# Kernel tuning notes

Measured on AMD Instinct MI355X. Metric: run time of the kernel, lower is better.

Reference implementation:

```python
import jax, jax.numpy as jnp
import numpy as np

B, T, L, V = 2048, 256, 32, 128
BLANK = V - 1          # Keras/TF CTC uses last class as blank
EPS = 1e-7             # keras backend epsilon used in ctc_batch_cost's log
NEG = -1e30            # log-space -inf surrogate (fp-safe)


def setup_inputs() -> dict:
    key = jax.random.key(0)
    k1, k2 = jax.random.split(key)
    # y_pred are softmax posteriors, as ctc_batch_cost expects
    logits = jax.random.normal(k1, (B, T, V), dtype=jnp.float32)
    y_pred = jax.nn.softmax(logits, axis=-1)
    # labels exclude the blank class (V-1)
    y_true = jax.random.randint(k2, (B, L), 0, BLANK, dtype=jnp.int64)
    return {"y_true": y_true, "y_pred": y_pred}


def _ctc_loss(y_true, y_pred):
    Bb, Tt, Vv = y_pred.shape
    Ll = y_true.shape[1]
    S = 2 * Ll + 1  # extended label length: blank-interleaved

    # extended labels: [blank, l1, blank, l2, ..., lL, blank]  -> [B, S]
    ext = jnp.full((Bb, S), BLANK, dtype=y_true.dtype).at[:, 1::2].set(y_true)

    logp = jnp.log(y_pred + EPS)  # [B, T, V], matches K.ctc_batch_cost
    # gather per-frame log-probs of each extended-label symbol: [B, T, S]
    lp_ext = jnp.take_along_axis(
        logp, jnp.broadcast_to(ext[:, None, :], (Bb, Tt, S)), axis=2
    )

    # skip transition (s-2 -> s) allowed iff ext[s] != blank and ext[s] != ext[s-2]
    ext_m2 = jnp.pad(ext, ((0, 0), (2, 0)), constant_values=-1)[:, :S]
    skip = (ext != BLANK) & (ext != ext_m2)  # [B, S]

    # alpha init at t=0: only first blank and first label reachable
    alpha0 = (
        jnp.full((Bb, S), NEG, dtype=logp.dtype)
        .at[:, 0].set(lp_ext[:, 0, 0])
        .at[:, 1].set(lp_ext[:, 0, 1])
    )

    def step(alpha, lp_t):
        # alpha: [B, S], lp_t: [B, S]
        s1 = jnp.pad(alpha, ((0, 0), (1, 0)), constant_values=NEG)[:, :S]
        s2 = jnp.pad(alpha, ((0, 0), (2, 0)), constant_values=NEG)[:, :S]
        a = jnp.logaddexp(alpha, s1)
        a = jnp.logaddexp(a, jnp.where(skip, s2, NEG))
        return a + lp_t, None

    lp_ts = jnp.transpose(lp_ext, (1, 0, 2))[1:]  # [T-1, B, S]
    alphaT, _ = jax.lax.scan(step, alpha0, lp_ts)

    # total log-likelihood = logsumexp over last blank and last label states
    loss = -jnp.logaddexp(alphaT[:, S - 1], alphaT[:, S - 2])  # [B]
    return loss[:, None]  # K.ctc_batch_cost returns [B, 1]


def reference(y_true, y_pred):
    return _ctc_loss(y_true, y_pred)
```

## Files before the change

kernel.cpp:

```cpp
#include <hip/hip_runtime.h>


constexpr int Bb = 2048;
constexpr int Tt = 256;
constexpr int Ll = 32;
constexpr int Vv = 128;
constexpr int BLANK = Vv - 1;
constexpr int PF = 16;
#define EPSF 1e-7f
#define NEGF -1e30f
#define LN2F 0.6931471805599453f

__device__ __forceinline__ float fexp2(float x) { return __builtin_amdgcn_exp2f(x); }
__device__ __forceinline__ float flog2(float x) { return __builtin_amdgcn_logf(x); }
__device__ __forceinline__ float rdlane(float v, int l) {
    return __uint_as_float(__builtin_amdgcn_readlane(__float_as_uint(v), l));
}
__device__ __forceinline__ float dpp_shr1(float old, float src) {
    return __int_as_float(__builtin_amdgcn_update_dpp(
        __float_as_int(old), __float_as_int(src), 0x138 ,
        0xf, 0xf, false));
}

__global__ __launch_bounds__(256) void ctc_fwd(const int* __restrict__ y_true,
                                               const float* __restrict__ y_pred,
                                               float* __restrict__ out) {
    const int w    = blockIdx.x * 4 + (threadIdx.x >> 6);
    const int lane = threadIdx.x & 63;

    int sym = BLANK;
    if (!(lane & 1)) sym = y_true[w * Ll + (lane >> 1)];
    const int  symm2 = __shfl_up(sym, 2);
    const bool skip  = !(lane & 1) && (lane >= 2) && (sym != symm2);

    const float* rp = y_pred + (size_t)w * Tt * Vv + sym;

    const float lp20 = flog2(rp[0] + EPSF);
    float b0 = rdlane(lp20, 1);
    float m  = (lane == 0) ? lp20 : NEGF;
    float p  = 1.0f;
    const float negv = NEGF;
    const float onev = 1.0f;

    auto step = [&](float prob) {
        const float lp2  = flog2(prob + EPSF);
        const float lpb  = rdlane(lp2, 1);
        const float b0p  = b0;
        const float m1g = dpp_shr1(b0p,  m);
        const float p1g = dpp_shr1(onev, p);
        const float m2s = dpp_shr1(negv, m1g);
        const float p2g = dpp_shr1(onev, p1g);
        const float m2g = skip ? m2s : NEGF;
        const float hi  = fmaxf(fmaxf(m, m1g), m2g);
        const float pn  = p   * fexp2(m   - hi)
                        + p1g * fexp2(m1g - hi)
                        + p2g * fexp2(m2g - hi);
        m  = hi + lp2;
        p  = pn;
        b0 = b0p + lpb;
    };
    auto renorm = [&]() {
        m += flog2(fmaxf(p, 1e-30f));  p = 1.0f;
    };

    float buf[PF];
#pragma unroll
    for (int i = 0; i < PF; ++i) buf[i] = rp[(size_t)(1 + i) * Vv];

    for (int tb = 1; tb + PF <= Tt; tb += PF) {
#pragma unroll
        for (int i = 0; i < PF; ++i) {
            const float pr = buf[i];
            const int   tn = tb + i + PF;
            if (tn < Tt) buf[i] = rp[(size_t)tn * Vv];
            step(pr);
            if ((i & 7) == 7) renorm();
        }
    }
#pragma unroll
    for (int i = 0; i < PF - 1; ++i) {
        step(buf[i]);
        if (i == 7) renorm();
    }

    const float afin = m + flog2(fmaxf(p, 1e-30f));
    const float aA = rdlane(afin, 62);
    const float aB = rdlane(afin, 63);
    if (lane == 0) {
        const float h = fmaxf(aA, aB);
        const float r = h + flog2(fexp2(aA - h) + fexp2(aB - h));
        out[w] = -r * LN2F;
    }
}

extern "C" void kernel_launch(void* const* d_in, const int* in_sizes, int n_in,
                              void* d_out, int out_size, void* d_ws, size_t ws_size,
                              hipStream_t stream) {
    const int*   y_true = (const int*)d_in[0];
    const float* y_pred = (const float*)d_in[1];
    float*       out    = (float*)d_out;
    ctc_fwd<<<dim3(Bb / 4), dim3(256), 0, stream>>>(y_true, y_pred, out);
}
```

Measured before the change: 47.66 us.

## Split each sequence into producer and consumer waves with an LDS double buffer

Each block now handles one batch element with two waves. Wave 0 loads the posteriors, takes their log2 and writes 16-frame chunks into a double-buffered LDS array. Wave 1 reads each chunk after a barrier and runs only the DPP-based alpha recurrence. The aim is to take global-load latency and the log computation off the serial recurrence path. In exchange the kernel launches twice as many waves, half of which do no recurrence work, and adds a block barrier per chunk.

```diff
diff --git a/kernel.cpp b/kernel.cpp
--- a/kernel.cpp
+++ b/kernel.cpp
@@ -6,7 +6,8 @@
 constexpr int Ll = 32;
 constexpr int Vv = 128;
 constexpr int BLANK = Vv - 1;
-constexpr int PF = 16;
+constexpr int CHUNK = 16;
+constexpr int NCH = Tt / CHUNK;
 #define EPSF 1e-7f
 #define NEGF -1e30f
 #define LN2F 0.6931471805599453f
@@ -22,74 +23,99 @@
         0xf, 0xf, false));
 }
 
-__global__ __launch_bounds__(256) void ctc_fwd(const int* __restrict__ y_true,
+__global__ __launch_bounds__(128) void ctc_fwd(const int* __restrict__ y_true,
                                                const float* __restrict__ y_pred,
                                                float* __restrict__ out) {
-    const int w    = blockIdx.x * 4 + (threadIdx.x >> 6);
+    const int w    = blockIdx.x;
+    const int wave = threadIdx.x >> 6;
     const int lane = threadIdx.x & 63;
+
+    __shared__ float buf[2][CHUNK][64];
 
     int sym = BLANK;
     if (!(lane & 1)) sym = y_true[w * Ll + (lane >> 1)];
-    const int  symm2 = __shfl_up(sym, 2);
-    const bool skip  = !(lane & 1) && (lane >= 2) && (sym != symm2);
 
-    const float* rp = y_pred + (size_t)w * Tt * Vv + sym;
+    if (wave == 0) {
+        const float* rp = y_pred + (size_t)w * Tt * Vv + sym;
+        float rA[CHUNK], rB[CHUNK];
+#pragma unroll
+        for (int i = 0; i < CHUNK; ++i) rA[i] = rp[(size_t)i * Vv];
+        for (int cc = 0; cc < NCH / 2; ++cc) {
+            const int c0 = 2 * cc, c1 = 2 * cc + 1;
+#pragma unroll
+            for (int i = 0; i < CHUNK; ++i)
+                rB[i] = rp[(size_t)(c1 * CHUNK + i) * Vv];
+#pragma unroll
+            for (int i = 0; i < CHUNK; ++i)
+                buf[0][i][lane] = flog2(rA[i] + EPSF);
+            __syncthreads();
+            if (c1 + 1 < NCH) {
+#pragma unroll
+                for (int i = 0; i < CHUNK; ++i)
+                    rA[i] = rp[(size_t)((c1 + 1) * CHUNK + i) * Vv];
+            }
+#pragma unroll
+            for (int i = 0; i < CHUNK; ++i)
+                buf[1][i][lane] = flog2(rB[i] + EPSF);
+            __syncthreads();
+        }
+    } else {
+        const int  symm2 = __shfl_up(sym, 2);
+        const bool skip  = !(lane & 1) && (lane >= 2) && (sym != symm2);
 
-    const float lp20 = flog2(rp[0] + EPSF);
-    float b0 = rdlane(lp20, 1);
-    float m  = (lane == 0) ? lp20 : NEGF;
-    float p  = 1.0f;
-    const float negv = NEGF;
-    const float onev = 1.0f;
+        float m = NEGF, p = 1.0f, b0 = 0.0f;
 
-    auto step = [&](float prob) {
-        const float lp2  = flog2(prob + EPSF);
-        const float lpb  = rdlane(lp2, 1);
-        const float b0p  = b0;
-        const float m1g = dpp_shr1(b0p,  m);
-        const float p1g = dpp_shr1(onev, p);
-        const float m2s = dpp_shr1(negv, m1g);
-        const float p2g = dpp_shr1(onev, p1g);
-        const float m2g = skip ? m2s : NEGF;
-        const float hi  = fmaxf(fmaxf(m, m1g), m2g);
-        const float pn  = p   * fexp2(m   - hi)
-                        + p1g * fexp2(m1g - hi)
-                        + p2g * fexp2(m2g - hi);
-        m  = hi + lp2;
-        p  = pn;
-        b0 = b0p + lpb;
-    };
-    auto renorm = [&]() {
-        m += flog2(fmaxf(p, 1e-30f));  p = 1.0f;
-    };
+        auto step = [&](float lp2) {
+            const float lpb = rdlane(lp2, 1);
+            const float b0p = b0;
+            const float m1g = dpp_shr1(b0p,  m);
+            const float p1g = dpp_shr1(1.0f, p);
+            const float m2s = dpp_shr1(NEGF, m1g);
+            const float p2g = dpp_shr1(1.0f, p1g);
+            const float m2g = skip ? m2s : NEGF;
+            const float hi  = fmaxf(fmaxf(m, m1g), m2g);
+            const float pn  = p   * fexp2(m   - hi)
+                            + p1g * fexp2(m1g - hi)
+                            + p2g * fexp2(m2g - hi);
+            m  = hi + lp2;
+            p  = pn;
+            b0 = b0p + lpb;
+        };
+        auto renorm = [&]() {
+            m += flog2(fmaxf(p, 1e-30f));  p = 1.0f;
+        };
 
-    float buf[PF];
+        for (int c = 0; c < NCH; ++c) {
+            __syncthreads();
+            float lp[CHUNK];
 #pragma unroll
-    for (int i = 0; i < PF; ++i) buf[i] = rp[(size_t)(1 + i) * Vv];
+            for (int i = 0; i < CHUNK; ++i) lp[i] = buf[c & 1][i][lane];
+            if (c == 0) {
+                b0 = rdlane(lp[0], 1);
+                m  = (lane == 0) ? lp[0] : NEGF;
+                p  = 1.0f;
+#pragma unroll
+                for (int i = 1; i < CHUNK; ++i) {
+                    step(lp[i]);
+                    if ((i & 7) == 7) renorm();
+                }
+            } else {
+#pragma unroll
+                for (int i = 0; i < CHUNK; ++i) {
+                    step(lp[i]);
+                    if ((i & 7) == 7) renorm();
+                }
+            }
+        }
 
-    for (int tb = 1; tb + PF <= Tt; tb += PF) {
-#pragma unroll
-        for (int i = 0; i < PF; ++i) {
-            const float pr = buf[i];
-            const int   tn = tb + i + PF;
-            if (tn < Tt) buf[i] = rp[(size_t)tn * Vv];
-            step(pr);
-            if ((i & 7) == 7) renorm();
+        const float afin = m + flog2(fmaxf(p, 1e-30f));
+        const float aA = rdlane(afin, 62);
+        const float aB = rdlane(afin, 63);
+        if (lane == 0) {
+            const float h = fmaxf(aA, aB);
+            const float r = h + flog2(fexp2(aA - h) + fexp2(aB - h));
+            out[w] = -r * LN2F;
         }
-    }
-#pragma unroll
-    for (int i = 0; i < PF - 1; ++i) {
-        step(buf[i]);
-        if (i == 7) renorm();
-    }
-
-    const float afin = m + flog2(fmaxf(p, 1e-30f));
-    const float aA = rdlane(afin, 62);
-    const float aB = rdlane(afin, 63);
-    if (lane == 0) {
-        const float h = fmaxf(aA, aB);
-        const float r = h + flog2(fexp2(aA - h) + fexp2(aB - h));
-        out[w] = -r * LN2F;
     }
 }
 
@@ -99,5 +125,5 @@
     const int*   y_true = (const int*)d_in[0];
     const float* y_pred = (const float*)d_in[1];
     float*       out    = (float*)d_out;
-    ctc_fwd<<<dim3(Bb / 4), dim3(256), 0, stream>>>(y_true, y_pred, out);
+    ctc_fwd<<<dim3(Bb), dim3(128), 0, stream>>>(y_true, y_pred, out);
 }
```

After: 46.66 us. -2.1%, faster.
